# Kernel optimization log

Measured on AMD Instinct MI355X. Metric: run time of the kernel, lower is better.

The kernel has to match this reference:

```python
import jax, jax.numpy as jnp
import numpy as np

B = 256          # batch
C = 1024         # d_in / d_out
S = 14           # spacial_dim
H = 8            # heads
DK = 64          # d_k
DV = 64          # d_v
N = S * S + 1    # tokens incl. mean token (197)
CONV_CH = [8, 32, 64, 128, 256, 1024]
EPS = 1e-5


def setup_inputs() -> dict:
    key = jax.random.key(0)
    ks = iter(jax.random.split(key, 32))
    d = {}
    d['feature_map'] = jax.random.normal(next(ks), (B, C, S, S), jnp.float32)
    d['loss_map'] = jax.random.normal(next(ks), (B, CONV_CH[0], S, S), jnp.float32)
    # 1x1 conv weights stored as (out_ch, in_ch)
    for i in range(5):
        cin, cout = CONV_CH[i], CONV_CH[i + 1]
        d[f'w{i+1}'] = jax.random.normal(next(ks), (cout, cin), jnp.float32) / np.sqrt(cin).astype(np.float32)
        d[f'b{i+1}'] = jnp.zeros((cout,), jnp.float32)
    # attention projections (torch Linear layout: (out, in)), xavier-ish scale
    for name, (o, i_) in [('wq', (H * DK, C)), ('wk', (H * DK, C)), ('wv', (H * DV, C)), ('wo', (C, H * DV))]:
        d[name] = jax.random.normal(next(ks), (o, i_), jnp.float32) * np.sqrt(2.0 / (o + i_)).astype(np.float32)
        d['b' + name[1]] = jnp.zeros((o,), jnp.float32)
    d['ln_g'] = jnp.ones((C,), jnp.float32)
    d['ln_b'] = jnp.zeros((C,), jnp.float32)
    d['pos_kv'] = jax.random.normal(next(ks), (N, C), jnp.float32) / np.sqrt(C).astype(np.float32)
    d['pos_q'] = jax.random.normal(next(ks), (N, C), jnp.float32) / np.sqrt(C).astype(np.float32)
    return d


def _conv1x1(x, w, b):
    # x: (b, cin, h, w); w: (cout, cin)
    return jnp.einsum('bchw,oc->bohw', x, w) + b[None, :, None, None]


def _tokens(m):
    # (b, c, h, w) -> (b, h*w, c) with prepended mean token -> (b, h*w+1, c)
    b = m.shape[0]
    t = m.reshape(b, m.shape[1], -1).transpose(0, 2, 1)
    return jnp.concatenate([t.mean(axis=1, keepdims=True), t], axis=1)


def reference(feature_map, loss_map, w1, b1, w2, b2, w3, b3, w4, b4, w5, b5,
              wq, bq, wk, bk, wv, bv, wo, bo, ln_g, ln_b, pos_kv, pos_q):
    b = feature_map.shape[0]
    # 5-stage 1x1 conv chain (pure linear, no nonlinearity)
    lm = loss_map
    for w, bi in ((w1, b1), (w2, b2), (w3, b3), (w4, b4), (w5, b5)):
        lm = _conv1x1(lm, w, bi)
    x = _tokens(feature_map) + pos_kv[None]        # (b, N, C) keys/values
    lm_t = _tokens(lm) + pos_q[None]               # (b, N, C)
    queries = lm_t[:, :1]                          # (b, 1, C) single query
    # multi-head single-query cross-attention
    q = (queries @ wq.T + bq).reshape(b, 1, H, DK).transpose(0, 2, 1, 3)   # (b,h,1,dk)
    k = (x @ wk.T + bk).reshape(b, N, H, DK).transpose(0, 2, 1, 3)         # (b,h,N,dk)
    v = (x @ wv.T + bv).reshape(b, N, H, DV).transpose(0, 2, 1, 3)         # (b,h,N,dv)
    att = jnp.einsum('bhqd,bhkd->bhqk', q, k) / jnp.asarray(np.sqrt(DK), jnp.float32)
    w_att = jax.nn.softmax(att, axis=-1)
    out = jnp.einsum('bhqk,bhkd->bhqd', w_att, v).transpose(0, 2, 1, 3).reshape(b, 1, H * DV)
    out = out @ wo.T + bo                          # (b, 1, C)
    # residual + layernorm
    res = queries + out
    mu = res.mean(axis=-1, keepdims=True)
    var = ((res - mu) ** 2).mean(axis=-1, keepdims=True)
    out = (res - mu) * jax.lax.rsqrt(var + EPS) * ln_g + ln_b
    return out.squeeze(1)                          # (b, C)
```

## Files before the change

### kernel.cpp

```cpp
#include <hip/hip_runtime.h>

#define WS_WC     ((size_t)0)
#define WS_BCQ    ((size_t)8192)
#define WS_WQP    ((size_t)9216)
#define WS_BQP    ((size_t)13312)
#define WS_U      ((size_t)13824)
#define WS_V      ((size_t)13888)
#define WS_P0     ((size_t)13896)
#define WS_P0C    ((size_t)13960)
#define WS_PS     ((size_t)13968)
#define WS_PSC    ((size_t)14032)
#define WS_G      ((size_t)14336)
#define WS_G0     ((size_t)79872)
#define WS_POST   ((size_t)88064)
#define WS_PSUM   ((size_t)301056)
#define WS_M0     ((size_t)302080)
#define WS_ATTP   ((size_t)304128)
#define WS_WFM    ((size_t)2008064)
#define WS_WPOS   ((size_t)2434048)
#define WS_S      ((size_t)2860032)
#define WS_OVP    ((size_t)4957184)
#define WS_O1P    ((size_t)6005760)
#define WS_POSTP  ((size_t)7054336)
#define WS_OV     ((size_t)7259136)
#define WS_M4     WS_S
#define WS_PP     WS_OVP

__global__ __launch_bounds__(256) void kp1a_chain_post(
    const float* __restrict__ w1, const float* __restrict__ b1,
    const float* __restrict__ w2, const float* __restrict__ b2,
    const float* __restrict__ w3, const float* __restrict__ b3,
    const float* __restrict__ w4, const float* __restrict__ b4,
    const float* __restrict__ pos_kv, float* __restrict__ ws)
{
  __shared__ float shm[12864];
  const int t = threadIdx.x;
  if (blockIdx.x == 0) {
    float* wt  = shm;
    float* M2s = shm + 8320;
    float* C2s = shm + 8832;
    float* M3s = shm + 8896;
    float* C3s = shm + 9920;
    float* M4s = shm + 10048;
    float* C4s = shm + 12096;

    for (int idx = t; idx < 2048; idx += 256) {
      const float4 v = ((const float4*)w3)[idx];
      const int r = idx >> 4, i = (idx & 15) * 4;
      float* d = &wt[r * 65 + i];
      d[0] = v.x; d[1] = v.y; d[2] = v.z; d[3] = v.w;
    }
    for (int idx = t; idx < 512; idx += 256) {
      const int o = idx >> 3, j = idx & 7;
      float a = 0.f;
      for (int i = 0; i < 32; ++i) a += w2[o*32+i] * w1[i*8+j];
      M2s[idx] = a;
    }
    if (t < 64) {
      float a = b2[t];
      for (int i = 0; i < 32; ++i) a += w2[t*32+i] * b1[i];
      C2s[t] = a;
    }
    __syncthreads();
    for (int idx = t; idx < 1024; idx += 256) {
      const int o = idx >> 3, j = idx & 7;
      const float* wr = &wt[o * 65];
      float a = 0.f;
      for (int i = 0; i < 64; ++i) a += wr[i] * M2s[i*8+j];
      M3s[idx] = a;
    }
    if (t < 128) {
      const float* wr = &wt[t * 65];
      float a = b3[t];
      for (int i = 0; i < 64; ++i) a += wr[i] * C2s[i];
      C3s[t] = a;
    }
    __syncthreads();
    for (int oc = 0; oc < 4; ++oc) {
      for (int idx = t; idx < 2048; idx += 256) {
        const float4 v = ((const float4*)w4)[oc*2048 + idx];
        const int r = idx >> 5, i = (idx & 31) * 4;
        float* d = &wt[r * 129 + i];
        d[0] = v.x; d[1] = v.y; d[2] = v.z; d[3] = v.w;
      }
      __syncthreads();
      for (int idx = t; idx < 512; idx += 256) {
        const int r = idx >> 3, j = idx & 7;
        const float* wr = &wt[r * 129];
        float a = 0.f;
        for (int i = 0; i < 128; ++i) a += wr[i] * M3s[i*8+j];
        M4s[(oc*64 + r)*8 + j] = a;
      }
      if (t < 64) {
        const float* wr = &wt[t * 129];
        float a = b4[oc*64 + t];
        for (int i = 0; i < 128; ++i) a += wr[i] * C3s[i];
        C4s[oc*64 + t] = a;
      }
      __syncthreads();
    }
    for (int idx = t; idx < 2048; idx += 256) ws[WS_M4 + idx] = M4s[idx];
    ws[WS_M4 + 2048 + t] = C4s[t];
  } else {
    const int c0 = (blockIdx.x - 1) * 64;
    const int c = t & 63, nb = t >> 6;
    for (int n = nb; n < 197; n += 4)
      shm[c*201 + n] = pos_kv[(size_t)n*1024 + c0 + c];
    __syncthreads();
    for (int idx = t; idx < 64*208; idx += 256) {
      int cc = idx / 208, n = idx - cc*208;
      ws[WS_POST + (size_t)(c0+cc)*208 + n] = (n < 197) ? shm[cc*201+n] : 0.f;
    }
    for (int idx = t; idx < 64*196; idx += 256) {
      int cc = idx / 196, p = idx - cc*196;
      ws[WS_POSTP + (size_t)(c0+cc)*200 + p] = shm[cc*201 + p + 1];
    }
    if (t < 64) {
      float s = 0.f;
      for (int n = 1; n < 197; ++n) s += shm[t*201 + n];
      ws[WS_PSUM + c0 + t] = s;
    }
  }
}

__global__ __launch_bounds__(256) void kp1b_w5fold(
    const float* __restrict__ w5, const float* __restrict__ b5,
    const float* __restrict__ pos_q, float* __restrict__ ws)
{
  __shared__ float wt[32 * 257];
  __shared__ float M4s[2304];
  const int t = threadIdx.x, ob = blockIdx.x;
  const int o0 = ob * 32;
  for (int idx = t; idx < 2304; idx += 256) M4s[idx] = ws[WS_M4 + idx];
  for (int idx = t; idx < 2048; idx += 256) {
    const float4 v = ((const float4*)w5)[(size_t)ob*2048 + idx];
    const int r = idx >> 6, i = (idx & 63) * 4;
    float* d = &wt[r * 257 + i];
    d[0] = v.x; d[1] = v.y; d[2] = v.z; d[3] = v.w;
  }
  __syncthreads();
  const int r = t >> 3, j = t & 7;
  const float* wr = &wt[r * 257];
  float a = 0.f;
  for (int i = 0; i < 256; ++i) a += wr[i] * M4s[i*8 + j];
  ws[WS_WC + (size_t)(o0 + r)*8 + j] = a;
  if (t < 32) {
    const float* wb = &wt[t * 257];
    float a2 = b5[o0 + t];
    for (int i = 0; i < 256; ++i) a2 += wb[i] * M4s[2048 + i];
    ws[WS_BCQ + o0 + t] = a2 + pos_q[o0 + t];
  }
}

__global__ __launch_bounds__(256) void kp2a_qproj(
    const float* __restrict__ wq, const float* __restrict__ bq,
    float* __restrict__ ws)
{
  const int t = threadIdx.x;
  const int w = t >> 6, l = t & 63;
  const int o = blockIdx.x * 4 + w;
  const float* wqr = wq + (size_t)o * 1024;
  float acc[8] = {0,0,0,0,0,0,0,0};
  float accb = 0.f;
  for (int k = 0; k < 16; ++k) {
    const int c = l + 64*k;
    const float wv_ = wqr[c];
    const float4 a  = *(const float4*)&ws[WS_WC + (size_t)c*8];
    const float4 b2 = *(const float4*)&ws[WS_WC + (size_t)c*8 + 4];
    acc[0] += wv_*a.x;  acc[1] += wv_*a.y;  acc[2] += wv_*a.z;  acc[3] += wv_*a.w;
    acc[4] += wv_*b2.x; acc[5] += wv_*b2.y; acc[6] += wv_*b2.z; acc[7] += wv_*b2.w;
    accb += wv_ * ws[WS_BCQ + c];
  }
  for (int off = 32; off >= 1; off >>= 1) {
#pragma unroll
    for (int j = 0; j < 8; ++j) acc[j] += __shfl_xor(acc[j], off);
    accb += __shfl_xor(accb, off);
  }
  if (l == 0) {
#pragma unroll
    for (int j = 0; j < 8; ++j) ws[WS_WQP + (size_t)o*8 + j] = acc[j];
    ws[WS_BQP + o] = accb + bq[o];
  }
}

__global__ __launch_bounds__(256) void kp2b_gfold(
    const float* __restrict__ wk, const float* __restrict__ bk,
    const float* __restrict__ pos_kv, float* __restrict__ ws)
{
  const int ci = blockIdx.x, h = blockIdx.y, t = threadIdx.x;
  __shared__ float WQs[512];
  __shared__ float BQs[64];
  __shared__ float red2[18 * 256];
  for (int idx = t; idx < 512; idx += 256) WQs[idx] = ws[WS_WQP + (size_t)h*512 + idx];
  if (t < 64) BQs[t] = ws[WS_BQP + h*64 + t];
  __syncthreads();

  const int c = ci*256 + t;
  float accG[8] = {0,0,0,0,0,0,0,0};
  float accg0 = 0.f;
  const float* wkc = wk + (size_t)h*64*1024 + c;
  for (int d = 0; d < 64; ++d) {
    const float wkv = wkc[(size_t)d*1024];
    const float4 qa = *(const float4*)&WQs[d*8];
    const float4 qb = *(const float4*)&WQs[d*8+4];
    accG[0] += wkv*qa.x; accG[1] += wkv*qa.y; accG[2] += wkv*qa.z; accG[3] += wkv*qa.w;
    accG[4] += wkv*qb.x; accG[5] += wkv*qb.y; accG[6] += wkv*qb.z; accG[7] += wkv*qb.w;
    accg0 += wkv * BQs[d];
  }
  *(float4*)&ws[WS_G + ((size_t)h*1024 + c)*8 + 0] = make_float4(accG[0],accG[1],accG[2],accG[3]);
  *(float4*)&ws[WS_G + ((size_t)h*1024 + c)*8 + 4] = make_float4(accG[4],accG[5],accG[6],accG[7]);
  ws[WS_G0 + (size_t)h*1024 + c] = accg0;

  const float z0 = pos_kv[c];
  const float zs = ws[WS_PSUM + c];
#pragma unroll
  for (int j = 0; j < 8; ++j) {
    red2[j*256 + t]     = accG[j]*z0;
    red2[(8+j)*256 + t] = accG[j]*zs;
  }
  red2[16*256 + t] = accg0*z0;
  red2[17*256 + t] = accg0*zs;
  __syncthreads();
  for (int s2 = 128; s2 >= 1; s2 >>= 1) {
    if (t < s2) {
#pragma unroll
      for (int j = 0; j < 18; ++j) red2[j*256 + t] += red2[j*256 + t + s2];
    }
    __syncthreads();
  }
  if (t == 0) {
    float* pp = &ws[WS_PP + ((size_t)ci*8 + h)*18];
#pragma unroll
    for (int j = 0; j < 18; ++j) pp[j] = red2[j*256];
  }

  if (ci == 0) {
    __syncthreads();
    const float bkv = (t < 64) ? bk[h*64 + t] : 0.f;
#pragma unroll
    for (int j = 0; j < 8; ++j)
      red2[j*256 + t] = (t < 64) ? bkv * WQs[t*8 + j] : 0.f;
    red2[8*256 + t] = (t < 64) ? bkv * BQs[t] : 0.f;
    __syncthreads();
    for (int s2 = 128; s2 >= 1; s2 >>= 1) {
      if (t < s2) {
#pragma unroll
        for (int j = 0; j < 9; ++j) red2[j*256 + t] += red2[j*256 + t + s2];
      }
      __syncthreads();
    }
    if (t == 0) {
#pragma unroll
      for (int j = 0; j < 8; ++j) ws[WS_U + h*8 + j] = red2[j*256];
      ws[WS_V + h] = red2[8*256];
    }
  }
}

__global__ __launch_bounds__(256) void kp2c_fold(float* __restrict__ ws)
{
  const int t = threadIdx.x;
  if (t < 64) {
    const int h = t >> 3, j = t & 7;
    float s = 0.f;
    for (int ci = 0; ci < 4; ++ci) s += ws[WS_PP + ((size_t)ci*8 + h)*18 + j];
    ws[WS_P0 + t] = s;
  } else if (t < 128) {
    const int u = t - 64; const int h = u >> 3, j = u & 7;
    float s = 0.f;
    for (int ci = 0; ci < 4; ++ci) s += ws[WS_PP + ((size_t)ci*8 + h)*18 + 8 + j];
    ws[WS_PS + u] = s;
  } else if (t < 136) {
    const int h = t - 128;
    float s = 0.f;
    for (int ci = 0; ci < 4; ++ci) s += ws[WS_PP + ((size_t)ci*8 + h)*18 + 16];
    ws[WS_P0C + h] = s;
  } else if (t < 144) {
    const int h = t - 136;
    float s = 0.f;
    for (int ci = 0; ci < 4; ++ci) s += ws[WS_PP + ((size_t)ci*8 + h)*18 + 17];
    ws[WS_PSC + h] = s;
  }
}

__global__ __launch_bounds__(256) void ka_att(
    const float* __restrict__ fm, const float* __restrict__ lmap,
    float* __restrict__ ws)
{
  const int ci = blockIdx.x, b = blockIdx.y, t = threadIdx.x;
  __shared__ float qk[256 * 8];
  __shared__ float m0s[8];
  {
    const int ch = t >> 5, lp = t & 31;
    float s = 0.f;
    for (int p = lp; p < 196; p += 32) s += lmap[((size_t)b*8 + ch)*196 + p];
    for (int off = 16; off >= 1; off >>= 1) s += __shfl_xor(s, off);
    if (lp == 0) m0s[ch] = s * (1.f/196.f);
  }
  __syncthreads();
  float m0r[8];
#pragma unroll
  for (int j = 0; j < 8; ++j) m0r[j] = m0s[j];
  const int c0 = ci * 256;
  {
    const int c = c0 + t;
#pragma unroll
    for (int h = 0; h < 8; ++h) {
      const float* gr = &ws[WS_G + ((size_t)h*1024 + c)*8];
      const float4 ga = *(const float4*)gr;
      const float4 gb = *(const float4*)(gr + 4);
      qk[t*8 + h] = ws[WS_G0 + (size_t)h*1024 + c]
                  + ga.x*m0r[0] + ga.y*m0r[1] + ga.z*m0r[2] + ga.w*m0r[3]
                  + gb.x*m0r[4] + gb.y*m0r[5] + gb.z*m0r[6] + gb.w*m0r[7];
    }
  }
  if (ci == 0 && t < 8) ws[WS_M0 + (size_t)b*8 + t] = m0s[t];
  __syncthreads();
  if (t < 98) {
    float a0[8] = {0,0,0,0,0,0,0,0};
    float a1[8] = {0,0,0,0,0,0,0,0};
    const float* fmp = fm + ((size_t)b*1024 + c0)*196 + 2*t;
    const float* pp  = &ws[WS_POSTP + (size_t)c0*200 + 2*t];
    for (int cc = 0; cc < 256; ++cc) {
      const float2 f = *(const float2*)&fmp[(size_t)cc*196];
      const float2 g = *(const float2*)&pp[(size_t)cc*200];
      const float x0 = f.x + g.x, x1 = f.y + g.y;
      const float4 qa = *(const float4*)&qk[cc*8];
      const float4 qb = *(const float4*)&qk[cc*8 + 4];
      a0[0] += qa.x*x0; a1[0] += qa.x*x1;
      a0[1] += qa.y*x0; a1[1] += qa.y*x1;
      a0[2] += qa.z*x0; a1[2] += qa.z*x1;
      a0[3] += qa.w*x0; a1[3] += qa.w*x1;
      a0[4] += qb.x*x0; a1[4] += qb.x*x1;
      a0[5] += qb.y*x0; a1[5] += qb.y*x1;
      a0[6] += qb.z*x0; a1[6] += qb.z*x1;
      a0[7] += qb.w*x0; a1[7] += qb.w*x1;
    }
    float* ap = &ws[WS_ATTP + (((size_t)b*4 + ci)*8)*208 + 2*t];
#pragma unroll
    for (int h = 0; h < 8; ++h)
      *(float2*)&ap[h*208] = make_float2(a0[h], a1[h]);
  }
}

__global__ __launch_bounds__(256) void ksm_softmax(float* __restrict__ ws)
{
  const int b = blockIdx.x, t = threadIdx.x;
  __shared__ float red[256 * 9];
  float m0r[8];
#pragma unroll
  for (int j = 0; j < 8; ++j) m0r[j] = ws[WS_M0 + (size_t)b*8 + j];
  float qbk[8], qs0[8], qss[8];
#pragma unroll
  for (int h = 0; h < 8; ++h) {
    float s1 = ws[WS_V + h], s2 = ws[WS_P0C + h], s3 = ws[WS_PSC + h];
#pragma unroll
    for (int j = 0; j < 8; ++j) {
      const float m = m0r[j];
      s1 += ws[WS_U  + h*8 + j] * m;
      s2 += ws[WS_P0 + h*8 + j] * m;
      s3 += ws[WS_PS + h*8 + j] * m;
    }
    qbk[h] = s1; qs0[h] = s2; qss[h] = s3;
  }
  float a[8];
#pragma unroll
  for (int h = 0; h < 8; ++h) a[h] = 0.f;
  if (t < 196) {
#pragma unroll
    for (int h = 0; h < 8; ++h) {
      float s = 0.f;
      for (int ci = 0; ci < 4; ++ci)
        s += ws[WS_ATTP + (((size_t)b*4 + ci)*8 + h)*208 + t];
      a[h] = s;
    }
  }
#pragma unroll
  for (int h = 0; h < 8; ++h) red[t*9 + h] = a[h];
  __syncthreads();
  for (int s2 = 128; s2 >= 1; s2 >>= 1) {
    if (t < s2) {
#pragma unroll
      for (int h = 0; h < 8; ++h) red[t*9+h] += red[(t+s2)*9+h];
    }
    __syncthreads();
  }
  float fa[8], fa0[8];
#pragma unroll
  for (int h = 0; h < 8; ++h) {
    const float S1 = red[h];
    fa[h]  = (a[h] + qbk[h]) * 0.125f;
    const float a0r = (S1 - qss[h]) * (1.f/196.f) + qs0[h];
    fa0[h] = (a0r + qbk[h]) * 0.125f;
  }
  __syncthreads();
#pragma unroll
  for (int h = 0; h < 8; ++h) red[t*9+h] = (t < 196) ? fa[h] : -3.0e38f;
  __syncthreads();
  for (int s2 = 128; s2 >= 1; s2 >>= 1) {
    if (t < s2) {
#pragma unroll
      for (int h = 0; h < 8; ++h) red[t*9+h] = fmaxf(red[t*9+h], red[(t+s2)*9+h]);
    }
    __syncthreads();
  }
  float mh[8];
#pragma unroll
  for (int h = 0; h < 8; ++h) mh[h] = fmaxf(red[h], fa0[h]);
  __syncthreads();
  float eh[8], e0[8];
#pragma unroll
  for (int h = 0; h < 8; ++h) {
    eh[h] = (t < 196) ? __expf(fa[h] - mh[h]) : 0.f;
    e0[h] = __expf(fa0[h] - mh[h]);
    red[t*9+h] = eh[h];
  }
  __syncthreads();
  for (int s2 = 128; s2 >= 1; s2 >>= 1) {
    if (t < s2) {
#pragma unroll
      for (int h = 0; h < 8; ++h) red[t*9+h] += red[(t+s2)*9+h];
    }
    __syncthreads();
  }
#pragma unroll
  for (int h = 0; h < 8; ++h) {
    const float lh  = red[h] + e0[h];
    const float inv = 1.f / lh;
    const float w0  = e0[h] * inv;
    float* wfm = &ws[WS_WFM  + ((size_t)b*8 + h)*208];
    float* wpo = &ws[WS_WPOS + ((size_t)b*8 + h)*208];
    if (t < 196) {
      wfm[t]   = eh[h]*inv + w0*(1.f/196.f);
      wpo[t+1] = eh[h]*inv;
    } else if (t < 208) {
      wfm[t] = 0.f;
      if (t == 196) wpo[0] = w0;
      else          wpo[t] = 0.f;
    }
  }
}

__global__ __launch_bounds__(256) void kb_fm(
    const float* __restrict__ fm, float* __restrict__ ws)
{
  __shared__ float fms[64 * 224];
  __shared__ float wfs[1664];
  const int cj = blockIdx.x, b = blockIdx.y, t = threadIdx.x;
  const int c0 = cj * 64;
  const float4* src = (const float4*)(fm + ((size_t)b*1024 + c0)*196);
  for (int idx = t; idx < 3136; idx += 256) {
    const float4 v = src[idx];
    const int c = idx / 49, q = idx - c*49;
    *(float4*)&fms[c*224 + ((q ^ (c & 7)) << 2)] = v;
  }
  const float4* wsrc = (const float4*)&ws[WS_WFM + (size_t)b*1664];
  for (int idx = t; idx < 416; idx += 256) {
    *(float4*)&wfs[idx*4] = wsrc[idx];
  }
  __syncthreads();
  const int c = t & 63, hh = t >> 6;
  const int h0 = hh*2, h1 = h0+1;
  const int cx = (c & 7) << 2;
  const float* fr = &fms[c*224];
  const float* w0p = &wfs[h0*208];
  const float* w1p = &wfs[h1*208];
  float a0 = 0.f, a1 = 0.f;
#pragma unroll 7
  for (int p4 = 0; p4 < 49; ++p4) {
    const float4 f  = *(const float4*)&fr[((p4 << 2) ^ cx)];
    const float4 u0 = *(const float4*)&w0p[p4*4];
    const float4 u1 = *(const float4*)&w1p[p4*4];
    a0 += f.x*u0.x + f.y*u0.y + f.z*u0.z + f.w*u0.w;
    a1 += f.x*u1.x + f.y*u1.y + f.z*u1.z + f.w*u1.w;
  }
  ws[WS_S + ((size_t)h0*256 + b)*1024 + c0 + c] = a0;
  ws[WS_S + ((size_t)h1*256 + b)*1024 + c0 + c] = a1;
}

__global__ __launch_bounds__(256) void kb_pos(float* __restrict__ ws)
{
  __shared__ float As[64 * 108];
  __shared__ float Bs[64 * 108];
  const int ct = blockIdx.x, rt = blockIdx.y, t = threadIdx.x;
  const int c0 = ct*64, r0 = rt*64;
  const int bq = t >> 4, cq = t & 15;
  float acc[4][4] = {};
  for (int sub = 0; sub < 2; ++sub) {
    const int k0 = sub * 104;
    __syncthreads();
    for (int idx = t; idx < 1664; idx += 256) {
      const int r = idx / 26, q = idx - r*26;
      const float4 av = *(const float4*)&ws[WS_WPOS + (size_t)(r0 + r)*208 + k0 + q*4];
      float* da = &As[r*108 + q*4];
      da[0]=av.x; da[1]=av.y; da[2]=av.z; da[3]=av.w;
      const float4 bv = *(const float4*)&ws[WS_POST + (size_t)(c0 + r)*208 + k0 + q*4];
      float* db = &Bs[r*108 + q*4];
      db[0]=bv.x; db[1]=bv.y; db[2]=bv.z; db[3]=bv.w;
    }
    __syncthreads();
    for (int k4 = 0; k4 < 26; ++k4) {
      float4 av[4], bw[4];
#pragma unroll
      for (int i = 0; i < 4; ++i) av[i] = *(const float4*)&As[(bq + 16*i)*108 + k4*4];
#pragma unroll
      for (int j = 0; j < 4; ++j) bw[j] = *(const float4*)&Bs[(cq + 16*j)*108 + k4*4];
#pragma unroll
      for (int i = 0; i < 4; ++i)
#pragma unroll
        for (int j = 0; j < 4; ++j)
          acc[i][j] += av[i].x*bw[j].x + av[i].y*bw[j].y + av[i].z*bw[j].z + av[i].w*bw[j].w;
    }
  }
#pragma unroll
  for (int i = 0; i < 4; ++i) {
    const int rIdx = r0 + bq + 16*i;
    const int b = rIdx >> 3, h = rIdx & 7;
    float* srow = &ws[WS_S + ((size_t)h*256 + b)*1024];
#pragma unroll
    for (int j = 0; j < 4; ++j) {
      const int c = c0 + cq + 16*j;
      srow[c] += acc[i][j];
    }
  }
}

__global__ __launch_bounds__(256) void kv_ov(
    const float* __restrict__ wv, float* __restrict__ ws)
{
  const int kt = blockIdx.x, bt = blockIdx.y, h = blockIdx.z, t = threadIdx.x;
  __shared__ float At[64 * 65];
  __shared__ float Bt[64 * 65];
  const int b0 = bt*64, k0 = kt*128;
  const int bq = t >> 4, dq = t & 15;
  float acc[4][4] = {};
  for (int sub = 0; sub < 2; ++sub) {
    const int kk0 = k0 + sub*64;
    __syncthreads();
    for (int r = 0; r < 4; ++r) {
      const int idx = t + 256*r;
      const int bi = idx >> 4, c4 = idx & 15;
      const float4 v = *(const float4*)&ws[WS_S + ((size_t)h*256 + b0 + bi)*1024 + kk0 + c4*4];
      float* d1 = &At[bi*65 + c4*4];
      d1[0]=v.x; d1[1]=v.y; d1[2]=v.z; d1[3]=v.w;
      const float4 w = *(const float4*)&wv[(size_t)(h*64 + bi)*1024 + kk0 + c4*4];
      float* d2 = &Bt[bi*65 + c4*4];
      d2[0]=w.x; d2[1]=w.y; d2[2]=w.z; d2[3]=w.w;
    }
    __syncthreads();
    for (int kk = 0; kk < 64; ++kk) {
      float av[4], bw[4];
#pragma unroll
      for (int i = 0; i < 4; ++i) av[i] = At[(bq*4+i)*65 + kk];
#pragma unroll
      for (int j = 0; j < 4; ++j) bw[j] = Bt[(dq*4+j)*65 + kk];
#pragma unroll
      for (int i = 0; i < 4; ++i)
#pragma unroll
        for (int j = 0; j < 4; ++j) acc[i][j] += av[i]*bw[j];
    }
  }
#pragma unroll
  for (int i = 0; i < 4; ++i) {
    *(float4*)&ws[WS_OVP + ((size_t)kt*256 + b0 + bq*4 + i)*512 + h*64 + dq*4] =
        make_float4(acc[i][0], acc[i][1], acc[i][2], acc[i][3]);
  }
}

__global__ __launch_bounds__(256) void kor_ovred(
    const float* __restrict__ bv, float* __restrict__ ws)
{
  const int b = blockIdx.x, t = threadIdx.x;
  for (int j = t; j < 512; j += 256) {
    float s = bv[j];
    for (int kt = 0; kt < 8; ++kt)
      s += ws[WS_OVP + ((size_t)kt*256 + b)*512 + j];
    ws[WS_OV + (size_t)b*512 + j] = s;
  }
}

__global__ __launch_bounds__(256) void ko_out(
    const float* __restrict__ wo, float* __restrict__ ws)
{
  const int kt2 = blockIdx.x, ct = blockIdx.y, bt = blockIdx.z, t = threadIdx.x;
  __shared__ float At[64 * 65];
  __shared__ float Bt[64 * 65];
  const int b0 = bt*64, c0 = ct*64, j0 = kt2*128;
  const int bq = t >> 4, cq = t & 15;
  float acc[4][4] = {};
  for (int sub = 0; sub < 2; ++sub) {
    const int jj0 = j0 + sub*64;
    __syncthreads();
    for (int r = 0; r < 4; ++r) {
      const int idx = t + 256*r;
      const int bi = idx >> 4, j4 = idx & 15;
      const float4 p = *(const float4*)&ws[WS_OV + (size_t)(b0 + bi)*512 + jj0 + j4*4];
      float* d1 = &At[bi*65 + j4*4];
      d1[0]=p.x; d1[1]=p.y; d1[2]=p.z; d1[3]=p.w;
      const float4 w = *(const float4*)&wo[(size_t)(c0 + bi)*512 + jj0 + j4*4];
      float* d2 = &Bt[bi*65 + j4*4];
      d2[0]=w.x; d2[1]=w.y; d2[2]=w.z; d2[3]=w.w;
    }
    __syncthreads();
    for (int jj = 0; jj < 64; ++jj) {
      float av[4], bw[4];
#pragma unroll
      for (int i = 0; i < 4; ++i) av[i] = At[(bq*4+i)*65 + jj];
#pragma unroll
      for (int j = 0; j < 4; ++j) bw[j] = Bt[(cq*4+j)*65 + jj];
#pragma unroll
      for (int i = 0; i < 4; ++i)
#pragma unroll
        for (int j = 0; j < 4; ++j) acc[i][j] += av[i]*bw[j];
    }
  }
#pragma unroll
  for (int i = 0; i < 4; ++i) {
    *(float4*)&ws[WS_O1P + ((size_t)kt2*256 + b0 + bq*4 + i)*1024 + c0 + cq*4] =
        make_float4(acc[i][0], acc[i][1], acc[i][2], acc[i][3]);
  }
}

__global__ __launch_bounds__(256) void kln_final(
    const float* __restrict__ bo, const float* __restrict__ ln_g,
    const float* __restrict__ ln_b, const float* __restrict__ ws,
    float* __restrict__ out)
{
  const int b = blockIdx.x, t = threadIdx.x;
  __shared__ float rs[256], rq[256];
  float m0r[8];
#pragma unroll
  for (int j = 0; j < 8; ++j) m0r[j] = ws[WS_M0 + (size_t)b*8 + j];
  float r[4];
  float sum = 0.f, sumsq = 0.f;
  for (int k = 0; k < 4; ++k) {
    const int c = t + 256*k;
    float o1 = bo[c];
    for (int kt2 = 0; kt2 < 4; ++kt2)
      o1 += ws[WS_O1P + ((size_t)kt2*256 + b)*1024 + c];
    const float* wc = &ws[WS_WC + c*8];
    float qv = ws[WS_BCQ + c];
#pragma unroll
    for (int j = 0; j < 8; ++j) qv += wc[j]*m0r[j];
    const float res = qv + o1;
    r[k] = res; sum += res; sumsq += res*res;
  }
  rs[t] = sum; rq[t] = sumsq;
  __syncthreads();
  for (int s2 = 128; s2 >= 1; s2 >>= 1) {
    if (t < s2) { rs[t] += rs[t+s2]; rq[t] += rq[t+s2]; }
    __syncthreads();
  }
  const float mu  = rs[0] * (1.f/1024.f);
  const float var = rq[0] * (1.f/1024.f) - mu*mu;
  const float inv = rsqrtf(var + 1e-5f);
  for (int k = 0; k < 4; ++k) {
    const int c = t + 256*k;
    out[(size_t)b*1024 + c] = (r[k] - mu)*inv*ln_g[c] + ln_b[c];
  }
}

extern "C" void kernel_launch(void* const* d_in, const int* in_sizes, int n_in,
                              void* d_out, int out_size, void* d_ws, size_t ws_size,
                              hipStream_t stream)
{
  const float* fm   = (const float*)d_in[0];
  const float* lmap = (const float*)d_in[1];
  const float* w1 = (const float*)d_in[2];  const float* b1 = (const float*)d_in[3];
  const float* w2 = (const float*)d_in[4];  const float* b2 = (const float*)d_in[5];
  const float* w3 = (const float*)d_in[6];  const float* b3 = (const float*)d_in[7];
  const float* w4 = (const float*)d_in[8];  const float* b4 = (const float*)d_in[9];
  const float* w5 = (const float*)d_in[10]; const float* b5 = (const float*)d_in[11];
  const float* wq = (const float*)d_in[12]; const float* bq = (const float*)d_in[13];
  const float* wk = (const float*)d_in[14]; const float* bk = (const float*)d_in[15];
  const float* wv = (const float*)d_in[16]; const float* bv = (const float*)d_in[17];
  const float* wo = (const float*)d_in[18]; const float* bo = (const float*)d_in[19];
  const float* ln_g = (const float*)d_in[20]; const float* ln_b = (const float*)d_in[21];
  const float* pos_kv = (const float*)d_in[22]; const float* pos_q = (const float*)d_in[23];
  float* ws  = (float*)d_ws;
  float* out = (float*)d_out;

  kp1a_chain_post<<<dim3(17), dim3(256), 0, stream>>>(w1,b1,w2,b2,w3,b3,w4,b4,pos_kv,ws);
  kp1b_w5fold<<<dim3(32), dim3(256), 0, stream>>>(w5,b5,pos_q,ws);
  kp2a_qproj<<<dim3(128), dim3(256), 0, stream>>>(wq,bq,ws);
  kp2b_gfold<<<dim3(4,8), dim3(256), 0, stream>>>(wk,bk,pos_kv,ws);
  kp2c_fold<<<dim3(1), dim3(256), 0, stream>>>(ws);
  ka_att<<<dim3(4,256), dim3(256), 0, stream>>>(fm,lmap,ws);
  ksm_softmax<<<dim3(256), dim3(256), 0, stream>>>(ws);
  kb_fm<<<dim3(16,256), dim3(256), 0, stream>>>(fm,ws);
  kb_pos<<<dim3(16,32), dim3(256), 0, stream>>>(ws);
  kv_ov<<<dim3(8,4,8), dim3(256), 0, stream>>>(wv,ws);
  kor_ovred<<<dim3(256), dim3(256), 0, stream>>>(bv,ws);
  ko_out<<<dim3(4,16,4), dim3(256), 0, stream>>>(wo,ws);
  kln_final<<<dim3(256), dim3(256), 0, stream>>>(bo,ln_g,ln_b,ws,out);
}
```

Measured before the change: 233.2 us.

## Precompute batch-independent positional attention logits and shuffle-reduce softmax

Positional-embedding contributions to attention logits no longer come from adding pos_kv to the feature map per batch. They are precomputed once, independent of batch, in a new kaj_pfold kernel as per-head, per-token coefficients that are combined with the m0 means inside the softmax. The att kernel now streams only the feature map, with a finer channel split (8×128 instead of 4×256). The softmax block reductions move from shared-memory tree reductions to wavefront shuffles plus a small cross-wave step. This removes redundant per-batch positional loads and some barriers, at the cost of more partial buffers for the softmax kernel to read.

Measured after the change: 288.2 us. +23.6%, slower.

```diff
diff --git a/kernel.cpp b/kernel.cpp
--- a/kernel.cpp
+++ b/kernel.cpp
@@ -6,23 +6,18 @@
 #define WS_BQP    ((size_t)13312)
 #define WS_U      ((size_t)13824)
 #define WS_V      ((size_t)13888)
-#define WS_P0     ((size_t)13896)
-#define WS_P0C    ((size_t)13960)
-#define WS_PS     ((size_t)13968)
-#define WS_PSC    ((size_t)14032)
 #define WS_G      ((size_t)14336)
 #define WS_G0     ((size_t)79872)
 #define WS_POST   ((size_t)88064)
-#define WS_PSUM   ((size_t)301056)
 #define WS_M0     ((size_t)302080)
-#define WS_ATTP   ((size_t)304128)
+#define WS_AJ     ((size_t)304128)
 #define WS_WFM    ((size_t)2008064)
 #define WS_WPOS   ((size_t)2434048)
 #define WS_S      ((size_t)2860032)
 #define WS_OVP    ((size_t)4957184)
 #define WS_O1P    ((size_t)6005760)
-#define WS_POSTP  ((size_t)7054336)
 #define WS_OV     ((size_t)7259136)
+#define WS_ATT8   ((size_t)7390208)
 #define WS_M4     WS_S
 #define WS_PP     WS_OVP
 
@@ -111,15 +106,6 @@
       int cc = idx / 208, n = idx - cc*208;
       ws[WS_POST + (size_t)(c0+cc)*208 + n] = (n < 197) ? shm[cc*201+n] : 0.f;
     }
-    for (int idx = t; idx < 64*196; idx += 256) {
-      int cc = idx / 196, p = idx - cc*196;
-      ws[WS_POSTP + (size_t)(c0+cc)*200 + p] = shm[cc*201 + p + 1];
-    }
-    if (t < 64) {
-      float s = 0.f;
-      for (int n = 1; n < 197; ++n) s += shm[t*201 + n];
-      ws[WS_PSUM + c0 + t] = s;
-    }
   }
 }
 
@@ -190,7 +176,7 @@
   const int ci = blockIdx.x, h = blockIdx.y, t = threadIdx.x;
   __shared__ float WQs[512];
   __shared__ float BQs[64];
-  __shared__ float red2[18 * 256];
+  __shared__ float red2[9 * 256];
   for (int idx = t; idx < 512; idx += 256) WQs[idx] = ws[WS_WQP + (size_t)h*512 + idx];
   if (t < 64) BQs[t] = ws[WS_BQP + h*64 + t];
   __syncthreads();
@@ -212,26 +198,21 @@
   ws[WS_G0 + (size_t)h*1024 + c] = accg0;
 
   const float z0 = pos_kv[c];
-  const float zs = ws[WS_PSUM + c];
-#pragma unroll
-  for (int j = 0; j < 8; ++j) {
-    red2[j*256 + t]     = accG[j]*z0;
-    red2[(8+j)*256 + t] = accG[j]*zs;
-  }
-  red2[16*256 + t] = accg0*z0;
-  red2[17*256 + t] = accg0*zs;
+#pragma unroll
+  for (int j = 0; j < 8; ++j) red2[j*256 + t] = accG[j]*z0;
+  red2[8*256 + t] = accg0*z0;
   __syncthreads();
   for (int s2 = 128; s2 >= 1; s2 >>= 1) {
     if (t < s2) {
 #pragma unroll
-      for (int j = 0; j < 18; ++j) red2[j*256 + t] += red2[j*256 + t + s2];
+      for (int j = 0; j < 9; ++j) red2[j*256 + t] += red2[j*256 + t + s2];
     }
     __syncthreads();
   }
   if (t == 0) {
-    float* pp = &ws[WS_PP + ((size_t)ci*8 + h)*18];
-#pragma unroll
-    for (int j = 0; j < 18; ++j) pp[j] = red2[j*256];
+    float* pp = &ws[WS_PP + ((size_t)ci*8 + h)*9];
+#pragma unroll
+    for (int j = 0; j < 9; ++j) pp[j] = red2[j*256];
   }
 
   if (ci == 0) {
@@ -257,30 +238,38 @@
   }
 }
 
-__global__ __launch_bounds__(256) void kp2c_fold(float* __restrict__ ws)
-{
-  const int t = threadIdx.x;
-  if (t < 64) {
-    const int h = t >> 3, j = t & 7;
-    float s = 0.f;
-    for (int ci = 0; ci < 4; ++ci) s += ws[WS_PP + ((size_t)ci*8 + h)*18 + j];
-    ws[WS_P0 + t] = s;
-  } else if (t < 128) {
-    const int u = t - 64; const int h = u >> 3, j = u & 7;
-    float s = 0.f;
-    for (int ci = 0; ci < 4; ++ci) s += ws[WS_PP + ((size_t)ci*8 + h)*18 + 8 + j];
-    ws[WS_PS + u] = s;
-  } else if (t < 136) {
-    const int h = t - 128;
-    float s = 0.f;
-    for (int ci = 0; ci < 4; ++ci) s += ws[WS_PP + ((size_t)ci*8 + h)*18 + 16];
-    ws[WS_P0C + h] = s;
-  } else if (t < 144) {
-    const int h = t - 136;
-    float s = 0.f;
-    for (int ci = 0; ci < 4; ++ci) s += ws[WS_PP + ((size_t)ci*8 + h)*18 + 17];
-    ws[WS_PSC + h] = s;
-  }
+__global__ __launch_bounds__(256) void kaj_pfold(float* __restrict__ ws)
+{
+  const int blk = blockIdx.x, t = threadIdx.x;
+  if (t >= 208) return;
+  const int h = blk / 9, j = blk - h*9;
+  float acc = 0.f;
+  if (t < 196) {
+    if (j < 8) {
+      const float* gp = &ws[WS_G + (size_t)h*1024*8 + j];
+      const float* pp = &ws[WS_POST + t];
+      float a0=0.f,a1=0.f,a2=0.f,a3=0.f;
+      for (int c = 0; c < 1024; c += 4) {
+        a0 += gp[(size_t)(c+0)*8] * pp[(size_t)(c+0)*208];
+        a1 += gp[(size_t)(c+1)*8] * pp[(size_t)(c+1)*208];
+        a2 += gp[(size_t)(c+2)*8] * pp[(size_t)(c+2)*208];
+        a3 += gp[(size_t)(c+3)*8] * pp[(size_t)(c+3)*208];
+      }
+      acc = (a0+a1)+(a2+a3);
+    } else {
+      const float* gp = &ws[WS_G0 + (size_t)h*1024];
+      const float* pp = &ws[WS_POST + t];
+      float a0=0.f,a1=0.f,a2=0.f,a3=0.f;
+      for (int c = 0; c < 1024; c += 4) {
+        a0 += gp[c+0] * pp[(size_t)(c+0)*208];
+        a1 += gp[c+1] * pp[(size_t)(c+1)*208];
+        a2 += gp[c+2] * pp[(size_t)(c+2)*208];
+        a3 += gp[c+3] * pp[(size_t)(c+3)*208];
+      }
+      acc = (a0+a1)+(a2+a3);
+    }
+  }
+  ws[WS_AJ + ((size_t)h*9 + j)*208 + t] = acc;
 }
 
 __global__ __launch_bounds__(256) void ka_att(
@@ -288,7 +277,7 @@
     float* __restrict__ ws)
 {
   const int ci = blockIdx.x, b = blockIdx.y, t = threadIdx.x;
-  __shared__ float qk[256 * 8];
+  __shared__ float qk[128 * 8];
   __shared__ float m0s[8];
   {
     const int ch = t >> 5, lp = t & 31;
@@ -301,8 +290,8 @@
   float m0r[8];
 #pragma unroll
   for (int j = 0; j < 8; ++j) m0r[j] = m0s[j];
-  const int c0 = ci * 256;
-  {
+  const int c0 = ci * 128;
+  if (t < 128) {
     const int c = c0 + t;
 #pragma unroll
     for (int h = 0; h < 8; ++h) {
@@ -320,23 +309,20 @@
     float a0[8] = {0,0,0,0,0,0,0,0};
     float a1[8] = {0,0,0,0,0,0,0,0};
     const float* fmp = fm + ((size_t)b*1024 + c0)*196 + 2*t;
-    const float* pp  = &ws[WS_POSTP + (size_t)c0*200 + 2*t];
-    for (int cc = 0; cc < 256; ++cc) {
+    for (int cc = 0; cc < 128; ++cc) {
       const float2 f = *(const float2*)&fmp[(size_t)cc*196];
-      const float2 g = *(const float2*)&pp[(size_t)cc*200];
-      const float x0 = f.x + g.x, x1 = f.y + g.y;
       const float4 qa = *(const float4*)&qk[cc*8];
       const float4 qb = *(const float4*)&qk[cc*8 + 4];
-      a0[0] += qa.x*x0; a1[0] += qa.x*x1;
-      a0[1] += qa.y*x0; a1[1] += qa.y*x1;
-      a0[2] += qa.z*x0; a1[2] += qa.z*x1;
-      a0[3] += qa.w*x0; a1[3] += qa.w*x1;
-      a0[4] += qb.x*x0; a1[4] += qb.x*x1;
-      a0[5] += qb.y*x0; a1[5] += qb.y*x1;
-      a0[6] += qb.z*x0; a1[6] += qb.z*x1;
-      a0[7] += qb.w*x0; a1[7] += qb.w*x1;
-    }
-    float* ap = &ws[WS_ATTP + (((size_t)b*4 + ci)*8)*208 + 2*t];
+      a0[0] += qa.x*f.x; a1[0] += qa.x*f.y;
+      a0[1] += qa.y*f.x; a1[1] += qa.y*f.y;
+      a0[2] += qa.z*f.x; a1[2] += qa.z*f.y;
+      a0[3] += qa.w*f.x; a1[3] += qa.w*f.y;
+      a0[4] += qb.x*f.x; a1[4] += qb.x*f.y;
+      a0[5] += qb.y*f.x; a1[5] += qb.y*f.y;
+      a0[6] += qb.z*f.x; a1[6] += qb.z*f.y;
+      a0[7] += qb.w*f.x; a1[7] += qb.w*f.y;
+    }
+    float* ap = &ws[WS_ATT8 + (((size_t)b*8 + ci)*8)*208 + 2*t];
 #pragma unroll
     for (int h = 0; h < 8; ++h)
       *(float2*)&ap[h*208] = make_float2(a0[h], a1[h]);
@@ -346,86 +332,113 @@
 __global__ __launch_bounds__(256) void ksm_softmax(float* __restrict__ ws)
 {
   const int b = blockIdx.x, t = threadIdx.x;
-  __shared__ float red[256 * 9];
+  __shared__ float wredA[32], wredB[32], wredC[32];
+  const int wv_ = t >> 6;
   float m0r[8];
 #pragma unroll
   for (int j = 0; j < 8; ++j) m0r[j] = ws[WS_M0 + (size_t)b*8 + j];
-  float qbk[8], qs0[8], qss[8];
+  float qbk[8], qs0[8];
 #pragma unroll
   for (int h = 0; h < 8; ++h) {
-    float s1 = ws[WS_V + h], s2 = ws[WS_P0C + h], s3 = ws[WS_PSC + h];
-#pragma unroll
-    for (int j = 0; j < 8; ++j) {
-      const float m = m0r[j];
-      s1 += ws[WS_U  + h*8 + j] * m;
-      s2 += ws[WS_P0 + h*8 + j] * m;
-      s3 += ws[WS_PS + h*8 + j] * m;
-    }
-    qbk[h] = s1; qs0[h] = s2; qss[h] = s3;
-  }
-  float a[8];
-#pragma unroll
-  for (int h = 0; h < 8; ++h) a[h] = 0.f;
+    float s1 = ws[WS_V + h];
+#pragma unroll
+    for (int j = 0; j < 8; ++j) s1 += ws[WS_U + h*8 + j] * m0r[j];
+    qbk[h] = s1;
+    float s2 = 0.f;
+    for (int ci = 0; ci < 4; ++ci) {
+      const float* pp = &ws[WS_PP + ((size_t)ci*8 + h)*9];
+      float v = pp[8];
+#pragma unroll
+      for (int j = 0; j < 8; ++j) v += pp[j]*m0r[j];
+      s2 += v;
+    }
+    qs0[h] = s2;
+  }
+  float a[8] = {0,0,0,0,0,0,0,0};
   if (t < 196) {
 #pragma unroll
     for (int h = 0; h < 8; ++h) {
       float s = 0.f;
-      for (int ci = 0; ci < 4; ++ci)
-        s += ws[WS_ATTP + (((size_t)b*4 + ci)*8 + h)*208 + t];
+      for (int ci = 0; ci < 8; ++ci)
+        s += ws[WS_ATT8 + (((size_t)b*8 + ci)*8 + h)*208 + t];
       a[h] = s;
     }
   }
-#pragma unroll
-  for (int h = 0; h < 8; ++h) red[t*9 + h] = a[h];
-  __syncthreads();
-  for (int s2 = 128; s2 >= 1; s2 >>= 1) {
-    if (t < s2) {
-#pragma unroll
-      for (int h = 0; h < 8; ++h) red[t*9+h] += red[(t+s2)*9+h];
-    }
-    __syncthreads();
-  }
+  {
+    float r[8];
+#pragma unroll
+    for (int h = 0; h < 8; ++h) r[h] = a[h];
+    for (int off = 32; off >= 1; off >>= 1) {
+#pragma unroll
+      for (int h = 0; h < 8; ++h) r[h] += __shfl_xor(r[h], off);
+    }
+    if ((t & 63) == 0) {
+#pragma unroll
+      for (int h = 0; h < 8; ++h) wredA[wv_*8 + h] = r[h];
+    }
+  }
+  float pa[8];
+#pragma unroll
+  for (int h = 0; h < 8; ++h) pa[h] = 0.f;
+  if (t < 196) {
+#pragma unroll
+    for (int h = 0; h < 8; ++h) {
+      const float* aj = &ws[WS_AJ + (size_t)h*9*208];
+      float v = aj[8*208 + t];
+#pragma unroll
+      for (int j = 0; j < 8; ++j) v += aj[j*208 + t]*m0r[j];
+      pa[h] = v;
+    }
+  }
+  __syncthreads();
   float fa[8], fa0[8];
 #pragma unroll
   for (int h = 0; h < 8; ++h) {
-    const float S1 = red[h];
-    fa[h]  = (a[h] + qbk[h]) * 0.125f;
-    const float a0r = (S1 - qss[h]) * (1.f/196.f) + qs0[h];
-    fa0[h] = (a0r + qbk[h]) * 0.125f;
-  }
-  __syncthreads();
-#pragma unroll
-  for (int h = 0; h < 8; ++h) red[t*9+h] = (t < 196) ? fa[h] : -3.0e38f;
-  __syncthreads();
-  for (int s2 = 128; s2 >= 1; s2 >>= 1) {
-    if (t < s2) {
-#pragma unroll
-      for (int h = 0; h < 8; ++h) red[t*9+h] = fmaxf(red[t*9+h], red[(t+s2)*9+h]);
-    }
-    __syncthreads();
-  }
+    const float S1 = wredA[h] + wredA[8+h] + wredA[16+h] + wredA[24+h];
+    fa[h]  = (a[h] + pa[h] + qbk[h]) * 0.125f;
+    fa0[h] = (S1*(1.f/196.f) + qs0[h] + qbk[h]) * 0.125f;
+  }
+  {
+    float r[8];
+#pragma unroll
+    for (int h = 0; h < 8; ++h) r[h] = (t < 196) ? fa[h] : -3.0e38f;
+    for (int off = 32; off >= 1; off >>= 1) {
+#pragma unroll
+      for (int h = 0; h < 8; ++h) r[h] = fmaxf(r[h], __shfl_xor(r[h], off));
+    }
+    if ((t & 63) == 0) {
+#pragma unroll
+      for (int h = 0; h < 8; ++h) wredB[wv_*8 + h] = r[h];
+    }
+  }
+  __syncthreads();
   float mh[8];
 #pragma unroll
-  for (int h = 0; h < 8; ++h) mh[h] = fmaxf(red[h], fa0[h]);
-  __syncthreads();
+  for (int h = 0; h < 8; ++h)
+    mh[h] = fmaxf(fmaxf(fmaxf(wredB[h], wredB[8+h]), fmaxf(wredB[16+h], wredB[24+h])), fa0[h]);
   float eh[8], e0[8];
 #pragma unroll
   for (int h = 0; h < 8; ++h) {
     eh[h] = (t < 196) ? __expf(fa[h] - mh[h]) : 0.f;
     e0[h] = __expf(fa0[h] - mh[h]);
-    red[t*9+h] = eh[h];
-  }
-  __syncthreads();
-  for (int s2 = 128; s2 >= 1; s2 >>= 1) {
-    if (t < s2) {
-#pragma unroll
-      for (int h = 0; h < 8; ++h) red[t*9+h] += red[(t+s2)*9+h];
-    }
-    __syncthreads();
-  }
+  }
+  {
+    float r[8];
+#pragma unroll
+    for (int h = 0; h < 8; ++h) r[h] = eh[h];
+    for (int off = 32; off >= 1; off >>= 1) {
+#pragma unroll
+      for (int h = 0; h < 8; ++h) r[h] += __shfl_xor(r[h], off);
+    }
+    if ((t & 63) == 0) {
+#pragma unroll
+      for (int h = 0; h < 8; ++h) wredC[wv_*8 + h] = r[h];
+    }
+  }
+  __syncthreads();
 #pragma unroll
   for (int h = 0; h < 8; ++h) {
-    const float lh  = red[h] + e0[h];
+    const float lh  = wredC[h] + wredC[8+h] + wredC[16+h] + wredC[24+h] + e0[h];
     const float inv = 1.f / lh;
     const float w0  = e0[h] * inv;
     float* wfm = &ws[WS_WFM  + ((size_t)b*8 + h)*208];
@@ -684,8 +697,8 @@
   kp1b_w5fold<<<dim3(32), dim3(256), 0, stream>>>(w5,b5,pos_q,ws);
   kp2a_qproj<<<dim3(128), dim3(256), 0, stream>>>(wq,bq,ws);
   kp2b_gfold<<<dim3(4,8), dim3(256), 0, stream>>>(wk,bk,pos_kv,ws);
-  kp2c_fold<<<dim3(1), dim3(256), 0, stream>>>(ws);
-  ka_att<<<dim3(4,256), dim3(256), 0, stream>>>(fm,lmap,ws);
+  ka_att<<<dim3(8,256), dim3(256), 0, stream>>>(fm,lmap,ws);
+  kaj_pfold<<<dim3(72), dim3(256), 0, stream>>>(ws);
   ksm_softmax<<<dim3(256), dim3(256), 0, stream>>>(ws);
   kb_fm<<<dim3(16,256), dim3(256), 0, stream>>>(fm,ws);
   kb_pos<<<dim3(16,32), dim3(256), 0, stream>>>(ws);
```

## Split attention-score channel loop across both thread halves and drop fold kernel

Applied to the files above, without the earlier changes.

The ka_att kernel previously used only 98 of 256 threads to loop over 256 channels. It now splits the channel range between two 128-thread halves and combines the partial sums through shared memory, which roughly doubles active lanes and halves the serial loop length. Separately, the tiny single-block kp2c_fold launch is removed, and its partial-sum reduction is recomputed inline in ksm_softmax by every thread. This saves one kernel launch and its serialization at the cost of some redundant loads per softmax block.

After: 225.9 us. 3.1% less time.

```diff
diff --git a/kernel.cpp b/kernel.cpp
--- a/kernel.cpp
+++ b/kernel.cpp
@@ -6,10 +6,6 @@
 #define WS_BQP    ((size_t)13312)
 #define WS_U      ((size_t)13824)
 #define WS_V      ((size_t)13888)
-#define WS_P0     ((size_t)13896)
-#define WS_P0C    ((size_t)13960)
-#define WS_PS     ((size_t)13968)
-#define WS_PSC    ((size_t)14032)
 #define WS_G      ((size_t)14336)
 #define WS_G0     ((size_t)79872)
 #define WS_POST   ((size_t)88064)
@@ -257,38 +253,13 @@
   }
 }
 
-__global__ __launch_bounds__(256) void kp2c_fold(float* __restrict__ ws)
-{
-  const int t = threadIdx.x;
-  if (t < 64) {
-    const int h = t >> 3, j = t & 7;
-    float s = 0.f;
-    for (int ci = 0; ci < 4; ++ci) s += ws[WS_PP + ((size_t)ci*8 + h)*18 + j];
-    ws[WS_P0 + t] = s;
-  } else if (t < 128) {
-    const int u = t - 64; const int h = u >> 3, j = u & 7;
-    float s = 0.f;
-    for (int ci = 0; ci < 4; ++ci) s += ws[WS_PP + ((size_t)ci*8 + h)*18 + 8 + j];
-    ws[WS_PS + u] = s;
-  } else if (t < 136) {
-    const int h = t - 128;
-    float s = 0.f;
-    for (int ci = 0; ci < 4; ++ci) s += ws[WS_PP + ((size_t)ci*8 + h)*18 + 16];
-    ws[WS_P0C + h] = s;
-  } else if (t < 144) {
-    const int h = t - 136;
-    float s = 0.f;
-    for (int ci = 0; ci < 4; ++ci) s += ws[WS_PP + ((size_t)ci*8 + h)*18 + 17];
-    ws[WS_PSC + h] = s;
-  }
-}
-
 __global__ __launch_bounds__(256) void ka_att(
     const float* __restrict__ fm, const float* __restrict__ lmap,
     float* __restrict__ ws)
 {
   const int ci = blockIdx.x, b = blockIdx.y, t = threadIdx.x;
   __shared__ float qk[256 * 8];
+  __shared__ float pa[98 * 17];
   __shared__ float m0s[8];
   {
     const int ch = t >> 5, lp = t & 31;
@@ -316,17 +287,19 @@
   }
   if (ci == 0 && t < 8) ws[WS_M0 + (size_t)b*8 + t] = m0s[t];
   __syncthreads();
-  if (t < 98) {
-    float a0[8] = {0,0,0,0,0,0,0,0};
-    float a1[8] = {0,0,0,0,0,0,0,0};
-    const float* fmp = fm + ((size_t)b*1024 + c0)*196 + 2*t;
-    const float* pp  = &ws[WS_POSTP + (size_t)c0*200 + 2*t];
-    for (int cc = 0; cc < 256; ++cc) {
+  const int half = t >> 7, tl = t & 127;
+  float a0[8] = {0,0,0,0,0,0,0,0};
+  float a1[8] = {0,0,0,0,0,0,0,0};
+  if (tl < 98) {
+    const float* fmp = fm + ((size_t)b*1024 + c0 + half*128)*196 + 2*tl;
+    const float* pp  = &ws[WS_POSTP + (size_t)(c0 + half*128)*200 + 2*tl];
+    const float* qkh = &qk[half*128*8];
+    for (int cc = 0; cc < 128; ++cc) {
       const float2 f = *(const float2*)&fmp[(size_t)cc*196];
       const float2 g = *(const float2*)&pp[(size_t)cc*200];
       const float x0 = f.x + g.x, x1 = f.y + g.y;
-      const float4 qa = *(const float4*)&qk[cc*8];
-      const float4 qb = *(const float4*)&qk[cc*8 + 4];
+      const float4 qa = *(const float4*)&qkh[cc*8];
+      const float4 qb = *(const float4*)&qkh[cc*8 + 4];
       a0[0] += qa.x*x0; a1[0] += qa.x*x1;
       a0[1] += qa.y*x0; a1[1] += qa.y*x1;
       a0[2] += qa.z*x0; a1[2] += qa.z*x1;
@@ -336,10 +309,19 @@
       a0[6] += qb.z*x0; a1[6] += qb.z*x1;
       a0[7] += qb.w*x0; a1[7] += qb.w*x1;
     }
-    float* ap = &ws[WS_ATTP + (((size_t)b*4 + ci)*8)*208 + 2*t];
+  }
+  if (half == 1 && tl < 98) {
+    float* d = &pa[tl*17];
+#pragma unroll
+    for (int h = 0; h < 8; ++h) { d[h] = a0[h]; d[8+h] = a1[h]; }
+  }
+  __syncthreads();
+  if (half == 0 && tl < 98) {
+    const float* d = &pa[tl*17];
+    float* ap = &ws[WS_ATTP + (((size_t)b*4 + ci)*8)*208 + 2*tl];
 #pragma unroll
     for (int h = 0; h < 8; ++h)
-      *(float2*)&ap[h*208] = make_float2(a0[h], a1[h]);
+      *(float2*)&ap[h*208] = make_float2(a0[h] + d[h], a1[h] + d[8+h]);
   }
 }
 
@@ -353,15 +335,22 @@
   float qbk[8], qs0[8], qss[8];
 #pragma unroll
   for (int h = 0; h < 8; ++h) {
-    float s1 = ws[WS_V + h], s2 = ws[WS_P0C + h], s3 = ws[WS_PSC + h];
-#pragma unroll
-    for (int j = 0; j < 8; ++j) {
-      const float m = m0r[j];
-      s1 += ws[WS_U  + h*8 + j] * m;
-      s2 += ws[WS_P0 + h*8 + j] * m;
-      s3 += ws[WS_PS + h*8 + j] * m;
-    }
-    qbk[h] = s1; qs0[h] = s2; qss[h] = s3;
+    float s1 = ws[WS_V + h];
+#pragma unroll
+    for (int j = 0; j < 8; ++j) s1 += ws[WS_U + h*8 + j] * m0r[j];
+    qbk[h] = s1;
+    float s2 = 0.f, s3 = 0.f;
+    for (int ci = 0; ci < 4; ++ci) {
+      const float* pp = &ws[WS_PP + ((size_t)ci*8 + h)*18];
+      float v2 = pp[16], v3 = pp[17];
+#pragma unroll
+      for (int j = 0; j < 8; ++j) {
+        v2 += pp[j]   * m0r[j];
+        v3 += pp[8+j] * m0r[j];
+      }
+      s2 += v2; s3 += v3;
+    }
+    qs0[h] = s2; qss[h] = s3;
   }
   float a[8];
 #pragma unroll
@@ -684,7 +673,6 @@
   kp1b_w5fold<<<dim3(32), dim3(256), 0, stream>>>(w5,b5,pos_q,ws);
   kp2a_qproj<<<dim3(128), dim3(256), 0, stream>>>(wq,bq,ws);
   kp2b_gfold<<<dim3(4,8), dim3(256), 0, stream>>>(wk,bk,pos_kv,ws);
-  kp2c_fold<<<dim3(1), dim3(256), 0, stream>>>(ws);
   ka_att<<<dim3(4,256), dim3(256), 0, stream>>>(fm,lmap,ws);
   ksm_softmax<<<dim3(256), dim3(256), 0, stream>>>(ws);
   kb_fm<<<dim3(16,256), dim3(256), 0, stream>>>(fm,ws);
```
